# Kernel optimization log

Hardware: AMD Instinct MI355X
Metric: run time of the kernel (lower is better)

The kernel has to match this reference:

```python
import jax, jax.numpy as jnp
import numpy as np

B, S, H, E, F, TOP_K = 4, 2048, 512, 16, 1024, 2


def setup_inputs() -> dict:
    key = jax.random.key(0)
    k0, k1, k2, k3, k4 = jax.random.split(key, 5)
    scale = 0.02
    return {
        "inputs": jax.random.normal(k0, (B, S, H), dtype=jnp.float32),
        "router_w": jax.random.normal(k1, (E, H), dtype=jnp.float32) * scale,
        "gate_w": jax.random.normal(k2, (E, H, F), dtype=jnp.float32) * scale,
        "up_w": jax.random.normal(k3, (E, H, F), dtype=jnp.float32) * scale,
        "down_w": jax.random.normal(k4, (E, F, H), dtype=jnp.float32) * scale,
    }


def _moe_forward(inputs, router_w, gate_w, up_w, down_w):
    b, s, h = inputs.shape
    x = inputs.reshape(-1, h)                      # [T, H]
    T = x.shape[0]
    # --- routing: topk of logits then fp32 softmax over the k selected ---
    router_logits = x @ router_w.T                 # [T, E]
    top_vals, top_idx = jax.lax.top_k(router_logits, TOP_K)   # [T, K]
    weights = jax.nn.softmax(top_vals.astype(jnp.float32), axis=-1)  # [T, K]
    # dense combine weights: w[t, e] = routing weight if expert e selected else 0
    combine = jnp.zeros((T, router_w.shape[0]), jnp.float32)
    combine = combine.at[jnp.arange(T)[:, None], top_idx].set(weights)  # [T, E]

    # --- per-expert SwiGLU MLP, weighted combine (scan over experts) ---
    def step(acc, ew):
        wg, wu, wd, ce = ew                        # [H,F], [H,F], [F,H], [T]
        hid = jax.nn.silu(x @ wg) * (x @ wu)       # [T, F]
        y = hid @ wd                               # [T, H]
        return acc + ce[:, None] * y, None

    out0 = jnp.zeros_like(x)
    out, _ = jax.lax.scan(step, out0, (gate_w, up_w, down_w, combine.T))
    return out.reshape(b, s, h), router_logits, top_idx


def reference(inputs, router_w, gate_w, up_w, down_w):
    out, router_logits, selected_experts = _moe_forward(
        inputs, router_w, gate_w, up_w, down_w)
    return out
```

## Files before the change

### kernel.cpp

```cpp
#include <hip/hip_runtime.h>
#include <cstdint>
#include <cstddef>

#define T_TOK 8192
#define H_DIM 512
#define E_NUM 16
#define F_DIM 1024

typedef __bf16 bf16x8 __attribute__((ext_vector_type(8)));
typedef float f32x4 __attribute__((ext_vector_type(4)));

#define OFF_XBF  0UL
#define OFF_HID  8388608UL
#define OFF_GW   41943040UL
#define OFF_UW   58720256UL
#define OFF_DW   75497472UL
#define OFF_STOK 92274688UL
#define OFF_SW   92340224UL
#define OFF_TOPE 92405760UL
#define OFF_TOPW 92471296UL
#define OFF_CNT  92536832UL
#define OFF_CUR  92537856UL
#define OFF_OFFS 92538880UL
#define OFF_SIDX 92539904UL
#define OFF_L128 92605440UL
#define OFF_L64  92606464UL
#define OFF_YB   OFF_GW

__device__ __forceinline__ unsigned short f2bf(float f) {
  union { float f; uint32_t u; } v; v.f = f;
  uint32_t r = v.u + 0x7fffu + ((v.u >> 16) & 1u);
  return (unsigned short)(r >> 16);
}

__device__ __forceinline__ float bf2f(unsigned short u) {
  union { uint32_t u; float f; } v; v.u = (uint32_t)u << 16;
  return v.f;
}

__device__ __forceinline__ void gld16(const void* g, void* l) {
  __builtin_amdgcn_global_load_lds(
      (const __attribute__((address_space(1))) unsigned int*)g,
      (__attribute__((address_space(3))) unsigned int*)l, 16, 0, 0);
}

__global__ __launch_bounds__(256) void k_pre(
    const float* __restrict__ x, const float* __restrict__ rw,
    const float* __restrict__ gw, const float* __restrict__ uw,
    const float* __restrict__ dw,
    unsigned short* __restrict__ xbf, int* __restrict__ tope,
    float* __restrict__ topw,
    unsigned short* __restrict__ gws, unsigned short* __restrict__ uws,
    unsigned short* __restrict__ dws, int* __restrict__ counts) {
  const int bid = blockIdx.x;
  const int tid = threadIdx.x;
  __shared__ __align__(16) uint32_t lsu[4096];
  __shared__ int lh[E_NUM];

  if (bid < 3072) {
    const int isgu = (bid < 2048);
    const float* src;
    unsigned short* dst;
    size_t obase0;
    int ldn;
    int e, kc;
    if (isgu) {
      e = bid >> 7;
      const int mat = (bid >> 6) & 1;
      kc = (bid >> 2) & 15;
      const int f2 = bid & 3;
      src = (mat ? uw : gw) + (size_t)e * H_DIM * F_DIM + (size_t)kc * 32 * F_DIM + f2 * 256;
      dst = mat ? uws : gws;
      obase0 = (((size_t)e * 8 + f2 * 2) * 16 + kc) * 4096;
      ldn = F_DIM;
    } else {
      const int r = bid - 2048;
      e = r >> 6;
      kc = (r >> 1) & 31;
      const int ht = r & 1;
      src = dw + (size_t)e * F_DIM * H_DIM + (size_t)kc * 32 * H_DIM + ht * 256;
      dst = dws;
      obase0 = (((size_t)e * 2 + ht) * 32 + kc) * 8192;
      ldn = H_DIM;
    }
    const int nb = tid & 63, kb = tid >> 6;
    const float* s0 = src + (size_t)kb * 8 * ldn + nb * 4;
    float4 v[8];
    #pragma unroll
    for (int j = 0; j < 8; ++j) v[j] = *(const float4*)(s0 + (size_t)j * ldn);
    #pragma unroll
    for (int i = 0; i < 4; ++i) {
      const int n = nb * 4 + i;
      uint4 q;
      q.x = (uint32_t)f2bf(((const float*)&v[0])[i]) | ((uint32_t)f2bf(((const float*)&v[1])[i]) << 16);
      q.y = (uint32_t)f2bf(((const float*)&v[2])[i]) | ((uint32_t)f2bf(((const float*)&v[3])[i]) << 16);
      q.z = (uint32_t)f2bf(((const float*)&v[4])[i]) | ((uint32_t)f2bf(((const float*)&v[5])[i]) << 16);
      q.w = (uint32_t)f2bf(((const float*)&v[6])[i]) | ((uint32_t)f2bf(((const float*)&v[7])[i]) << 16);
      const int jr = n >> 1, sw = (jr ^ (jr >> 3)) & 7;
      const int ccs = (((n & 1) << 2) + kb) ^ sw;
      *(uint4*)&lsu[jr * 32 + ccs * 4] = q;
    }
    __syncthreads();
    const int n = tid;
    const int jr = n >> 1, sw = (jr ^ (jr >> 3)) & 7;
    #pragma unroll
    for (int c = 0; c < 4; ++c) {
      const int ccs = (((n & 1) << 2) + c) ^ sw;
      uint4 q = *(const uint4*)&lsu[jr * 32 + ccs * 4];
      if (isgu) {
        const int fi = n & 127, s = (c ^ fi) & 3;
        const size_t ob = obase0 + (size_t)(n >> 7) * 16 * 4096;
        *(uint4*)&dst[ob + fi * 32 + s * 8] = q;
      } else {
        const int s = (c ^ n) & 3;
        *(uint4*)&dst[obase0 + n * 32 + s * 8] = q;
      }
    }
  } else {
    if (tid < E_NUM) lh[tid] = 0;
    __syncthreads();
    const int rb = bid - 3072;
    const int wave = tid >> 6, lane = tid & 63;
    const int t = rb * 4 + wave;
    const float4* xr = (const float4*)(x + (size_t)t * H_DIM + lane * 8);
    float4 a = xr[0], b = xr[1];
    float xi[8] = {a.x, a.y, a.z, a.w, b.x, b.y, b.z, b.w};
    uint4 o;
    o.x = (uint32_t)f2bf(xi[0]) | ((uint32_t)f2bf(xi[1]) << 16);
    o.y = (uint32_t)f2bf(xi[2]) | ((uint32_t)f2bf(xi[3]) << 16);
    o.z = (uint32_t)f2bf(xi[4]) | ((uint32_t)f2bf(xi[5]) << 16);
    o.w = (uint32_t)f2bf(xi[6]) | ((uint32_t)f2bf(xi[7]) << 16);
    *(uint4*)(xbf + (size_t)t * H_DIM + lane * 8) = o;
    float acc[E_NUM];
    #pragma unroll
    for (int e = 0; e < E_NUM; ++e) {
      const float4* wr = (const float4*)(rw + e * H_DIM + lane * 8);
      float4 wa = wr[0], wb = wr[1];
      acc[e] = xi[0]*wa.x + xi[1]*wa.y + xi[2]*wa.z + xi[3]*wa.w
             + xi[4]*wb.x + xi[5]*wb.y + xi[6]*wb.z + xi[7]*wb.w;
    }
    #pragma unroll
    for (int off = 1; off < 64; off <<= 1) {
      #pragma unroll
      for (int e = 0; e < E_NUM; ++e) acc[e] += __shfl_xor(acc[e], off);
    }
    if (lane == 0) {
      int e0 = 0; float v0 = acc[0];
      #pragma unroll
      for (int e = 1; e < E_NUM; ++e) if (acc[e] > v0) { v0 = acc[e]; e0 = e; }
      int e1 = -1; float v1 = -3.4e38f;
      #pragma unroll
      for (int e = 0; e < E_NUM; ++e) if (e != e0 && acc[e] > v1) { v1 = acc[e]; e1 = e; }
      float ee = __expf(v1 - v0);
      float inv = 1.0f / (1.0f + ee);
      tope[t*2]   = e0; tope[t*2+1] = e1;
      topw[t*2]   = inv; topw[t*2+1] = ee * inv;
      atomicAdd(&lh[e0], 1);
      atomicAdd(&lh[e1], 1);
    }
    __syncthreads();
    if (tid < E_NUM && lh[tid] > 0) atomicAdd(&counts[tid * 16], lh[tid]);
  }
}

__global__ void k_offsets(const int* __restrict__ counts, int* __restrict__ offs,
                          int* __restrict__ list128, int* __restrict__ list64) {
  __shared__ int sc[16], b128[16], b64[16];
  if (threadIdx.x == 0) {
    int s = 0, a = 0, b = 0;
    for (int e = 0; e < E_NUM; ++e) {
      int c = counts[e * 16];
      sc[e] = c; b128[e] = a; b64[e] = b;
      offs[e] = s;
      s += c; a += (c + 127) >> 7; b += (c + 63) >> 6;
    }
    offs[16] = s; offs[18] = a; offs[19] = b;
  }
  __syncthreads();
  for (int e = 0; e < E_NUM; ++e) {
    const int n1 = (sc[e] + 127) >> 7;
    for (int ti = threadIdx.x; ti < n1; ti += 64) list128[b128[e] + ti] = (e << 24) | (ti << 7);
    const int n2 = (sc[e] + 63) >> 6;
    for (int ti = threadIdx.x; ti < n2; ti += 64) list64[b64[e] + ti] = (e << 24) | (ti << 6);
  }
}

__global__ __launch_bounds__(256) void k_scatter(
    const int* __restrict__ tope, const float* __restrict__ topw,
    const int* __restrict__ offs, int* __restrict__ cursors,
    int* __restrict__ stok, float* __restrict__ sw, int* __restrict__ sidx) {
  __shared__ int lh[E_NUM];
  __shared__ int lbase[E_NUM];
  const int tid = threadIdx.x;
  const int t = blockIdx.x * 256 + tid;
  if (tid < E_NUM) lh[tid] = 0;
  __syncthreads();
  int e0 = tope[t*2], e1 = tope[t*2+1];
  int r0 = atomicAdd(&lh[e0], 1);
  int r1 = atomicAdd(&lh[e1], 1);
  __syncthreads();
  if (tid < E_NUM) lbase[tid] = atomicAdd(&cursors[tid * 16], lh[tid]);
  __syncthreads();
  int s0 = offs[e0] + lbase[e0] + r0;
  int s1 = offs[e1] + lbase[e1] + r1;
  stok[s0] = t; sw[s0] = topw[t*2];
  stok[s1] = t; sw[s1] = topw[t*2+1];
  sidx[t*2] = s0; sidx[t*2+1] = s1;
}

__global__ __launch_bounds__(256, 2) void k_gateup(
    const unsigned short* __restrict__ xbf,
    const unsigned short* __restrict__ gws, const unsigned short* __restrict__ uws,
    const int* __restrict__ stok, const int* __restrict__ counts,
    const int* __restrict__ offs, const int* __restrict__ list128,
    unsigned short* __restrict__ hid) {
  const int y = blockIdx.y;
  if (y >= offs[18]) return;
  const int v = list128[y];
  const int e = v >> 24, t0 = v & 0xffffff;
  const int cnt = counts[e * 16];
  const int base = offs[e];
  const int fx = blockIdx.x;

  __shared__ __align__(16) unsigned short sb[2][3][4096];

  const int tid = threadIdx.x;
  const int wave = tid >> 6, lane = tid & 63;
  const int l15 = lane & 15, hi = lane >> 4;
  const int wm = wave >> 1, wn = wave & 1;

  const int r0 = tid >> 2, slot = tid & 3;
  const int rr0 = min(t0 + r0, cnt - 1), rr1 = min(t0 + r0 + 64, cnt - 1);
  const char* sA0 = (const char*)xbf + (size_t)stok[base + rr0] * 1024 + ((slot ^ (r0 & 3)) * 16);
  const char* sA1 = (const char*)xbf + (size_t)stok[base + rr1] * 1024 + ((slot ^ (r0 & 3)) * 16);
  const char* sG = (const char*)gws + (((size_t)e * 8 + fx) * 16) * 8192 + tid * 16;
  const char* sU = (const char*)uws + (((size_t)e * 8 + fx) * 16) * 8192 + tid * 16;
  unsigned short* const dA = &sb[0][0][wave * 512];
  unsigned short* const dG = &sb[0][1][wave * 512];
  unsigned short* const dU = &sb[0][2][wave * 512];
  const int bufo = 3 * 4096;

  f32x4 accg[4][4] = {}; f32x4 accu[4][4] = {};

  #define STAGE_GU(b, kk) { \
    gld16(sA0 + (kk)*64, dA + (b)*bufo); \
    gld16(sA1 + (kk)*64, dA + (b)*bufo + 2048); \
    gld16(sG + (size_t)(kk)*8192, dG + (b)*bufo); \
    gld16(sG + (size_t)(kk)*8192 + 4096, dG + (b)*bufo + 2048); \
    gld16(sU + (size_t)(kk)*8192, dU + (b)*bufo); \
    gld16(sU + (size_t)(kk)*8192 + 4096, dU + (b)*bufo + 2048); }

  STAGE_GU(0, 0);
  __syncthreads();
  #pragma unroll 1
  for (int kk = 0; kk < 16; ++kk) {
    const int cur = kk & 1;
    if (kk < 15) STAGE_GU(cur ^ 1, kk + 1);
    const unsigned short* lA = &sb[cur][0][0];
    const unsigned short* lG = &sb[cur][1][0];
    const unsigned short* lU = &sb[cur][2][0];
    bf16x8 a[4], bg[4], bu[4];
    #pragma unroll
    for (int m = 0; m < 4; ++m) {
      int row = wm*64 + m*16 + l15;
      a[m] = *(const bf16x8*)((const char*)lA + row*64 + (((hi ^ row) & 3) << 4));
    }
    #pragma unroll
    for (int s = 0; s < 4; ++s) {
      int row = wn*64 + s*16 + l15;
      int o = row*64 + (((hi ^ row) & 3) << 4);
      bg[s] = *(const bf16x8*)((const char*)lG + o);
      bu[s] = *(const bf16x8*)((const char*)lU + o);
    }
    #pragma unroll
    for (int m = 0; m < 4; ++m)
      #pragma unroll
      for (int s = 0; s < 4; ++s) {
        accg[m][s] = __builtin_amdgcn_mfma_f32_16x16x32_bf16(a[m], bg[s], accg[m][s], 0, 0, 0);
        accu[m][s] = __builtin_amdgcn_mfma_f32_16x16x32_bf16(a[m], bu[s], accu[m][s], 0, 0, 0);
      }
    __syncthreads();
  }
  #undef STAGE_GU

  #pragma unroll
  for (int m = 0; m < 4; ++m)
    #pragma unroll
    for (int r = 0; r < 4; ++r) {
      int row = t0 + wm*64 + m*16 + hi*4 + r;
      if (row < cnt) {
        #pragma unroll
        for (int s = 0; s < 4; ++s) {
          float g = accg[m][s][r], u = accu[m][s][r];
          float h = g / (1.0f + __expf(-g)) * u;
          hid[(size_t)(base + row) * 1024 + fx*128 + wn*64 + s*16 + l15] = f2bf(h);
        }
      }
    }
}

__global__ __launch_bounds__(256, 3) void k_down(
    const unsigned short* __restrict__ hid, const unsigned short* __restrict__ dws,
    const int* __restrict__ counts, const int* __restrict__ offs,
    const int* __restrict__ list64, unsigned short* __restrict__ ybuf) {
  const int y = blockIdx.y;
  if (y >= offs[19]) return;
  const int v = list64[y];
  const int e = v >> 24, t0 = v & 0xffffff;
  const int cnt = counts[e * 16];
  const int base = offs[e];
  const int ht = blockIdx.x;

  __shared__ __align__(16) unsigned short sbA[2][2048];
  __shared__ __align__(16) unsigned short sbW[2][8192];

  const int tid = threadIdx.x;
  const int wave = tid >> 6, lane = tid & 63;
  const int l15 = lane & 15, hi = lane >> 4;

  const int r0 = tid >> 2, slot = tid & 3;
  const int rr = min(t0 + r0, cnt - 1);
  const char* sA = (const char*)hid + (size_t)(base + rr) * 2048 + ((slot ^ (r0 & 3)) * 16);
  const char* sW = (const char*)dws + (((size_t)e * 2 + ht) * 32) * 16384 + tid * 16;
  unsigned short* const dA = &sbA[0][wave * 512];
  unsigned short* const dW = &sbW[0][wave * 512];

  f32x4 acc[4][4] = {};

  #define STAGE_DN(b, kk) { \
    gld16(sA + (kk)*64, dA + (b)*2048); \
    const char* w = sW + (size_t)(kk)*16384; \
    gld16(w,         dW + (b)*8192); \
    gld16(w + 4096,  dW + (b)*8192 + 2048); \
    gld16(w + 8192,  dW + (b)*8192 + 4096); \
    gld16(w + 12288, dW + (b)*8192 + 6144); }

  STAGE_DN(0, 0);
  __syncthreads();
  #pragma unroll 1
  for (int kk = 0; kk < 32; ++kk) {
    const int cur = kk & 1;
    if (kk < 31) STAGE_DN(cur ^ 1, kk + 1);
    const unsigned short* lA = &sbA[cur][0];
    const unsigned short* lW = &sbW[cur][0];
    bf16x8 a[4], b[4];
    #pragma unroll
    for (int m = 0; m < 4; ++m) {
      int row = m*16 + l15;
      a[m] = *(const bf16x8*)((const char*)lA + row*64 + (((hi ^ row) & 3) << 4));
    }
    #pragma unroll
    for (int s = 0; s < 4; ++s) {
      int row = wave*64 + s*16 + l15;
      b[s] = *(const bf16x8*)((const char*)lW + row*64 + (((hi ^ row) & 3) << 4));
    }
    #pragma unroll
    for (int m = 0; m < 4; ++m)
      #pragma unroll
      for (int s = 0; s < 4; ++s)
        acc[m][s] = __builtin_amdgcn_mfma_f32_16x16x32_bf16(a[m], b[s], acc[m][s], 0, 0, 0);
    __syncthreads();
  }
  #undef STAGE_DN

  #pragma unroll
  for (int m = 0; m < 4; ++m)
    #pragma unroll
    for (int r = 0; r < 4; ++r) {
      int row = t0 + m*16 + hi*4 + r;
      if (row < cnt) {
        unsigned short* yy = ybuf + (size_t)(base + row) * 512 + ht*256 + wave*64;
        #pragma unroll
        for (int s = 0; s < 4; ++s)
          yy[s*16 + l15] = f2bf(acc[m][s][r]);
      }
    }
}

__global__ __launch_bounds__(256) void k_gather(
    const unsigned short* __restrict__ ybuf, const int* __restrict__ sidx,
    const float* __restrict__ topw, float* __restrict__ out) {
  const int wave = threadIdx.x >> 6, lane = threadIdx.x & 63;
  const int t = blockIdx.x * 4 + wave;
  const int s0 = sidx[t*2], s1 = sidx[t*2+1];
  const float w0 = topw[t*2], w1 = topw[t*2+1];
  uint4 a = *(const uint4*)(ybuf + (size_t)s0 * 512 + lane * 8);
  uint4 b = *(const uint4*)(ybuf + (size_t)s1 * 512 + lane * 8);
  float4 o0, o1;
  o0.x = w0*bf2f((unsigned short)(a.x)) + w1*bf2f((unsigned short)(b.x));
  o0.y = w0*bf2f((unsigned short)(a.x>>16)) + w1*bf2f((unsigned short)(b.x>>16));
  o0.z = w0*bf2f((unsigned short)(a.y)) + w1*bf2f((unsigned short)(b.y));
  o0.w = w0*bf2f((unsigned short)(a.y>>16)) + w1*bf2f((unsigned short)(b.y>>16));
  o1.x = w0*bf2f((unsigned short)(a.z)) + w1*bf2f((unsigned short)(b.z));
  o1.y = w0*bf2f((unsigned short)(a.z>>16)) + w1*bf2f((unsigned short)(b.z>>16));
  o1.z = w0*bf2f((unsigned short)(a.w)) + w1*bf2f((unsigned short)(b.w));
  o1.w = w0*bf2f((unsigned short)(a.w>>16)) + w1*bf2f((unsigned short)(b.w>>16));
  float* orow = out + (size_t)t * H_DIM + lane * 8;
  *(float4*)orow = o0;
  *(float4*)(orow + 4) = o1;
}

extern "C" void kernel_launch(void* const* d_in, const int* in_sizes, int n_in,
                              void* d_out, int out_size, void* d_ws, size_t ws_size,
                              hipStream_t stream) {
  const float* x  = (const float*)d_in[0];
  const float* rw = (const float*)d_in[1];
  const float* gw = (const float*)d_in[2];
  const float* uw = (const float*)d_in[3];
  const float* dw = (const float*)d_in[4];
  float* out = (float*)d_out;
  char* ws = (char*)d_ws;

  unsigned short* xbf = (unsigned short*)(ws + OFF_XBF);
  unsigned short* hid = (unsigned short*)(ws + OFF_HID);
  unsigned short* gws = (unsigned short*)(ws + OFF_GW);
  unsigned short* uws = (unsigned short*)(ws + OFF_UW);
  unsigned short* dws = (unsigned short*)(ws + OFF_DW);
  unsigned short* ybuf = (unsigned short*)(ws + OFF_YB);
  int*   stok    = (int*)(ws + OFF_STOK);
  float* swt     = (float*)(ws + OFF_SW);
  int*   tope    = (int*)(ws + OFF_TOPE);
  float* topw    = (float*)(ws + OFF_TOPW);
  int*   counts  = (int*)(ws + OFF_CNT);
  int*   cursors = (int*)(ws + OFF_CUR);
  int*   offs    = (int*)(ws + OFF_OFFS);
  int*   sidx    = (int*)(ws + OFF_SIDX);
  int*   list128 = (int*)(ws + OFF_L128);
  int*   list64  = (int*)(ws + OFF_L64);

  hipMemsetAsync(ws + OFF_CNT, 0, 2048 + 128, stream);

  k_pre<<<5120, 256, 0, stream>>>(x, rw, gw, uw, dw, xbf, tope, topw, gws, uws, dws, counts);
  k_offsets<<<1, 64, 0, stream>>>(counts, offs, list128, list64);
  k_scatter<<<T_TOK / 256, 256, 0, stream>>>(tope, topw, offs, cursors, stok, swt, sidx);
  k_gateup<<<dim3(8, 160), 256, 0, stream>>>(
      xbf, gws, uws, stok, counts, offs, list128, hid);
  k_down<<<dim3(2, 288), 256, 0, stream>>>(
      hid, dws, counts, offs, list64, ybuf);
  k_gather<<<T_TOK / 4, 256, 0, stream>>>(ybuf, sidx, topw, out);
}
```

Before: 158.6 us.

## Repack weights and LDS tiles into MFMA-fragment order to drop XOR swizzle

```diff
diff --git a/kernel.cpp b/kernel.cpp
--- a/kernel.cpp
+++ b/kernel.cpp
@@ -101,19 +101,20 @@
       *(uint4*)&lsu[jr * 32 + ccs * 4] = q;
     }
     __syncthreads();
-    const int n = tid;
-    const int jr = n >> 1, sw = (jr ^ (jr >> 3)) & 7;
-    #pragma unroll
-    for (int c = 0; c < 4; ++c) {
-      const int ccs = (((n & 1) << 2) + c) ^ sw;
+    #pragma unroll
+    for (int j = 0; j < 4; ++j) {
+      const int li = tid + j * 256;
+      const int f  = ((li >> 6) << 4) | (li & 15);
+      const int kb2 = (li >> 4) & 3;
+      const int jr = f >> 1, sw2 = (jr ^ (jr >> 3)) & 7;
+      const int ccs = (((f & 1) << 2) + kb2) ^ sw2;
       uint4 q = *(const uint4*)&lsu[jr * 32 + ccs * 4];
       if (isgu) {
-        const int fi = n & 127, s = (c ^ fi) & 3;
-        const size_t ob = obase0 + (size_t)(n >> 7) * 16 * 4096;
-        *(uint4*)&dst[ob + fi * 32 + s * 8] = q;
+        const size_t ob = obase0 + (size_t)(f >> 7) * (16 * 4096);
+        const int fl = f & 127;
+        *(uint4*)&dst[ob + (size_t)((fl >> 4) * 512 + kb2 * 128 + (fl & 15) * 8)] = q;
       } else {
-        const int s = (c ^ n) & 3;
-        *(uint4*)&dst[obase0 + n * 32 + s * 8] = q;
+        *(uint4*)&dst[obase0 + (size_t)li * 8] = q;
       }
     }
   } else {
@@ -229,10 +230,10 @@
   const int l15 = lane & 15, hi = lane >> 4;
   const int wm = wave >> 1, wn = wave & 1;
 
-  const int r0 = tid >> 2, slot = tid & 3;
-  const int rr0 = min(t0 + r0, cnt - 1), rr1 = min(t0 + r0 + 64, cnt - 1);
-  const char* sA0 = (const char*)xbf + (size_t)stok[base + rr0] * 1024 + ((slot ^ (r0 & 3)) * 16);
-  const char* sA1 = (const char*)xbf + (size_t)stok[base + rr1] * 1024 + ((slot ^ (r0 & 3)) * 16);
+  const int rr0 = min(t0 + wave * 16 + l15, cnt - 1);
+  const int rr1 = min(t0 + 64 + wave * 16 + l15, cnt - 1);
+  const char* sA0 = (const char*)xbf + (size_t)stok[base + rr0] * 1024 + hi * 16;
+  const char* sA1 = (const char*)xbf + (size_t)stok[base + rr1] * 1024 + hi * 16;
   const char* sG = (const char*)gws + (((size_t)e * 8 + fx) * 16) * 8192 + tid * 16;
   const char* sU = (const char*)uws + (((size_t)e * 8 + fx) * 16) * 8192 + tid * 16;
   unsigned short* const dA = &sb[0][0][wave * 512];
@@ -261,16 +262,13 @@
     const unsigned short* lU = &sb[cur][2][0];
     bf16x8 a[4], bg[4], bu[4];
     #pragma unroll
-    for (int m = 0; m < 4; ++m) {
-      int row = wm*64 + m*16 + l15;
-      a[m] = *(const bf16x8*)((const char*)lA + row*64 + (((hi ^ row) & 3) << 4));
-    }
+    for (int m = 0; m < 4; ++m)
+      a[m] = *(const bf16x8*)((const char*)lA + (wm*4 + m)*1024 + hi*256 + l15*16);
     #pragma unroll
     for (int s = 0; s < 4; ++s) {
-      int row = wn*64 + s*16 + l15;
-      int o = row*64 + (((hi ^ row) & 3) << 4);
-      bg[s] = *(const bf16x8*)((const char*)lG + o);
-      bu[s] = *(const bf16x8*)((const char*)lU + o);
+      const int ob = (wn*4 + s)*1024 + hi*256 + l15*16;
+      bg[s] = *(const bf16x8*)((const char*)lG + ob);
+      bu[s] = *(const bf16x8*)((const char*)lU + ob);
     }
     #pragma unroll
     for (int m = 0; m < 4; ++m)
@@ -318,9 +316,8 @@
   const int wave = tid >> 6, lane = tid & 63;
   const int l15 = lane & 15, hi = lane >> 4;
 
-  const int r0 = tid >> 2, slot = tid & 3;
-  const int rr = min(t0 + r0, cnt - 1);
-  const char* sA = (const char*)hid + (size_t)(base + rr) * 2048 + ((slot ^ (r0 & 3)) * 16);
+  const int rr = min(t0 + wave * 16 + l15, cnt - 1);
+  const char* sA = (const char*)hid + (size_t)(base + rr) * 2048 + hi * 16;
   const char* sW = (const char*)dws + (((size_t)e * 2 + ht) * 32) * 16384 + tid * 16;
   unsigned short* const dA = &sbA[0][wave * 512];
   unsigned short* const dW = &sbW[0][wave * 512];
@@ -345,15 +342,11 @@
     const unsigned short* lW = &sbW[cur][0];
     bf16x8 a[4], b[4];
     #pragma unroll
-    for (int m = 0; m < 4; ++m) {
-      int row = m*16 + l15;
-      a[m] = *(const bf16x8*)((const char*)lA + row*64 + (((hi ^ row) & 3) << 4));
-    }
-    #pragma unroll
-    for (int s = 0; s < 4; ++s) {
-      int row = wave*64 + s*16 + l15;
-      b[s] = *(const bf16x8*)((const char*)lW + row*64 + (((hi ^ row) & 3) << 4));
-    }
+    for (int m = 0; m < 4; ++m)
+      a[m] = *(const bf16x8*)((const char*)lA + m*1024 + hi*256 + l15*16);
+    #pragma unroll
+    for (int s = 0; s < 4; ++s)
+      b[s] = *(const bf16x8*)((const char*)lW + (wave*4 + s)*1024 + hi*256 + l15*16);
     #pragma unroll
     for (int m = 0; m < 4; ++m)
       #pragma unroll
```

Result: faster. 154.0 us (-2.9%).
